# Optimization experiments

Hardware: AMD Instinct MI355X
Metric: run time of the kernel (lower is better)

The kernel has to match this reference:

```python
import jax, jax.numpy as jnp
import numpy as np

B, H, KVH, D = 32, 32, 8, 128
BS = 128                      # KV-cache block size
BLOCKS_PER_SEQ = 14
NB = B * BLOCKS_PER_SEQ       # 448 active blocks
NUM_CACHE_BLOCKS = 512
CTX = 13 * BS + 64            # 1728 tokens per sequence (incl. new decode token)
SCALE = 0.08838834764831845   # 1/sqrt(head_size)
NEG = -1e9


def _slopes(n):
    return (2.0 ** (-8.0 / n * np.arange(1, n + 1))).astype(np.float32)


def setup_inputs() -> dict:
    key = jax.random.key(0)
    ks = jax.random.split(key, 5)
    query = jax.random.normal(ks[0], (B, 1, H * D), dtype=jnp.float32)
    key_t = jax.random.normal(ks[1], (B, 1, KVH * D), dtype=jnp.float32)
    value = jax.random.normal(ks[2], (B, 1, KVH * D), dtype=jnp.float32)
    key_cache = jax.random.normal(ks[3], (NUM_CACHE_BLOCKS, BS, KVH, D), dtype=jnp.float32)
    value_cache = jax.random.normal(ks[4], (NUM_CACHE_BLOCKS, BS, KVH, D), dtype=jnp.float32)

    block_list = np.arange(NB, dtype=np.int32)                      # cache block id per active block (seq-major)
    block_groups = np.repeat(np.arange(B, dtype=np.int32), BLOCKS_PER_SEQ)
    block_mapping = np.zeros((NB, B), dtype=np.float32)             # one-hot block->batch map
    block_mapping[np.arange(NB), block_groups] = 1.0

    valid = CTX - 13 * BS                                           # 64 valid slots in last block
    block_bias = np.zeros((NB, BS), dtype=np.float32)
    last = np.arange(B) * BLOCKS_PER_SEQ + (BLOCKS_PER_SEQ - 1)
    block_bias[last, valid:] = NEG

    # alibi distances per kv slot: (kv_pos - (CTX-1)); zero on masked slots
    pos_in_seq = (np.tile(np.arange(BLOCKS_PER_SEQ), B)[:, None] * BS
                  + np.arange(BS)[None, :]).astype(np.float32)
    alibi_blocks = np.where(block_bias < 0, 0.0, pos_in_seq - float(CTX - 1)).astype(np.float32)

    block_indices = last.astype(np.int32)                           # write new token into last block
    block_offsets = np.full((B,), valid - 1, dtype=np.int32)

    return {"query": query, "key": key_t, "value": value,
            "key_cache": key_cache, "value_cache": value_cache,
            "block_list": jnp.asarray(block_list), "block_groups": jnp.asarray(block_groups),
            "block_mapping": jnp.asarray(block_mapping), "block_bias": jnp.asarray(block_bias),
            "block_indices": jnp.asarray(block_indices), "block_offsets": jnp.asarray(block_offsets),
            "alibi_blocks": jnp.asarray(alibi_blocks), "alibi_slopes": jnp.asarray(_slopes(H))}


def reference(query, key, value, key_cache, value_cache, block_list, block_groups,
              block_mapping, block_bias, block_indices, block_offsets,
              alibi_blocks, alibi_slopes):
    G = H // KVH                                                    # queries per kv head
    q = query.reshape(B, H, D)
    k_new = key.reshape(B, KVH, D)
    v_new = value.reshape(B, KVH, D)
    # KV-cache insertion of the new decode token (VLLMKVCache insert)
    key_cache = key_cache.at[block_indices, block_offsets].set(k_new)
    value_cache = value_cache.at[block_indices, block_offsets].set(v_new)
    # batch2block: replicate each sequence's query to its blocks via one-hot matmul
    q_blk = jnp.einsum('nb,bhd->nhd', block_mapping, SCALE * q).reshape(NB, KVH, G, D)
    k = key_cache[block_list]                                       # [NB, BS, KVH, D] paged fetch
    v = value_cache[block_list]
    attn = jnp.einsum('nkgd,nskd->nkgs', q_blk, k)                  # [NB, KVH, G, BS]
    # decode alibi bias: slopes * per-slot distance, grouped for GQA
    pos_bias = (alibi_blocks[:, None, :] * alibi_slopes[None, :, None]).reshape(NB, KVH, G, BS)
    attn = attn + pos_bias + block_bias[:, None, None, :]
    # grouped (per-sequence) numerically-stable softmax across blocks
    block_max = jnp.max(attn, axis=-1)                              # [NB, KVH, G]
    group_max = jax.ops.segment_max(block_max, block_groups, num_segments=B)
    m = jax.lax.stop_gradient(group_max[block_groups])
    p = jnp.exp(attn - m[..., None])
    block_sum = jnp.sum(p, axis=-1)                                 # [NB, KVH, G]
    o_blk = jnp.einsum('nkgs,nskd->nkgd', p, v)                     # [NB, KVH, G, D]
    # block2batch: accumulate block partials back per sequence
    o = jnp.einsum('nb,nkgd->bkgd', block_mapping, o_blk)
    s = jnp.einsum('nb,nkg->bkg', block_mapping, block_sum)
    out = o / s[..., None]
    return out.reshape(B, 1, H * D)
```

## Files before the change

kernel.cpp:

```cpp
#include <hip/hip_runtime.h>
#include <stdint.h>

#define B_    32
#define H_    32
#define KVH_  8
#define D_    128
#define BS_   128
#define BPS_  14
#define NB_   448
#define G_    4
#define CHUNK_ 32
#define SCALE_ 0.08838834764831845f

__device__ __forceinline__ void g2lds16(const float* gp, float* lp) {
  __builtin_amdgcn_global_load_lds(
      (__attribute__((address_space(1))) void*)gp,
      (__attribute__((address_space(3))) void*)lp,
      16, 0, 0);
}

__global__ __launch_bounds__(256, 4) void attn_part_kernel(
    const float* __restrict__ query,
    const float* __restrict__ knew, const float* __restrict__ vnew,
    const float* __restrict__ kc, const float* __restrict__ vc,
    const int* __restrict__ block_list, const int* __restrict__ block_groups,
    const float* __restrict__ block_bias, const float* __restrict__ alibi_blocks,
    const float* __restrict__ alibi_slopes,
    float* __restrict__ p_o, float* __restrict__ p_m, float* __restrict__ p_l) {
  __shared__ float smem[2 * CHUNK_ * D_];
  __shared__ float q_s[G_ * D_];
  __shared__ float attn_s[G_ * BS_];
  __shared__ float bias_s[BS_];
  __shared__ float alibi_s[BS_];

  const int bid = blockIdx.x;
  const int n = bid >> 3, kvh = bid & 7;
  const int t = threadIdx.x;
  const int lane = t & 63, wv = t >> 6;
  const int s_loc = lane & 31, dh = lane >> 5;

  const int cb = block_list[n];
  const int b  = block_groups[n];
  const bool is_last = (n % BPS_ == BPS_ - 1);
  const int nch = is_last ? 2 : 4;

  const float* kbase = kc + ((size_t)cb * BS_ * KVH_ + kvh) * D_;
  const float* vbase = vc + ((size_t)cb * BS_ * KVH_ + kvh) * D_;
  const float* knew_row = knew + ((size_t)b * KVH_ + kvh) * D_;
  const float* vnew_row = vnew + ((size_t)b * KVH_ + kvh) * D_;

  {
    int r = wv * 8;
    #pragma unroll
    for (int i = 0; i < 4; ++i) {
      const float* g = kbase + (size_t)(r + 2 * i + dh) * (KVH_ * D_) + s_loc * 4;
      g2lds16(g, smem + (r + 2 * i) * D_);
    }
  }
  if (t < 128) {
    float4 qv = *(const float4*)(query + (size_t)b * (H_ * D_) +
                                 (size_t)kvh * (G_ * D_) + (size_t)t * 4);
    qv.x *= SCALE_; qv.y *= SCALE_; qv.z *= SCALE_; qv.w *= SCALE_;
    ((float4*)q_s)[t] = qv;
  } else {
    int i = t - 128;
    bias_s[i]  = block_bias[(size_t)n * BS_ + i];
    alibi_s[i] = alibi_blocks[(size_t)n * BS_ + i];
  }
  const float slope = alibi_slopes[kvh * G_ + wv];
  __syncthreads();

  const int rot = s_loc & 15;

  for (int c = 0; c < nch; ++c) {
    if (c + 1 < nch) {
      float* dst = smem + ((c + 1) & 1) * (CHUNK_ * D_);
      int r = wv * 8;
      #pragma unroll
      for (int i = 0; i < 4; ++i) {
        int row = (c + 1) * CHUNK_ + r + 2 * i + dh;
        const float* g = (is_last && row == 63)
                             ? knew_row + s_loc * 4
                             : kbase + (size_t)row * (KVH_ * D_) + s_loc * 4;
        g2lds16(g, dst + (r + 2 * i) * D_);
      }
    }
    float acc = 0.f;
    const float4* kb = (const float4*)(smem + (c & 1) * (CHUNK_ * D_) + s_loc * D_ + dh * 64);
    const float4* qb = (const float4*)(q_s + wv * D_ + dh * 64);
    #pragma unroll
    for (int j = 0; j < 16; ++j) {
      int jj = (j + rot) & 15;
      float4 kvv = kb[jj];
      float4 qv = qb[jj];
      acc += kvv.x * qv.x + kvv.y * qv.y + kvv.z * qv.z + kvv.w * qv.w;
    }
    acc += __shfl_xor(acc, 32);
    if (lane < 32) {
      int s = c * CHUNK_ + s_loc;
      attn_s[wv * BS_ + s] = acc + slope * alibi_s[s] + bias_s[s];
    }
    __syncthreads();
  }

  {
    float a0 = attn_s[wv * BS_ + lane];
    float a1 = (nch == 4) ? attn_s[wv * BS_ + 64 + lane] : -1e30f;
    float mx = fmaxf(a0, a1);
    #pragma unroll
    for (int off = 32; off > 0; off >>= 1) mx = fmaxf(mx, __shfl_xor(mx, off));
    float p0 = __expf(a0 - mx);
    float p1 = __expf(a1 - mx);
    attn_s[wv * BS_ + lane] = p0;
    if (nch == 4) attn_s[wv * BS_ + 64 + lane] = p1;
    float sm = p0 + p1;
    #pragma unroll
    for (int off = 32; off > 0; off >>= 1) sm += __shfl_xor(sm, off);
    if (lane == 0) {
      p_m[(size_t)bid * G_ + wv] = mx;
      p_l[(size_t)bid * G_ + wv] = sm;
    }
  }
  __syncthreads();

  const int col4 = (lane & 31) * 4;
  const int group = wv * 2 + (lane >> 5);
  float4 acc4[G_];
  #pragma unroll
  for (int g = 0; g < G_; ++g) acc4[g] = make_float4(0.f, 0.f, 0.f, 0.f);

  if (group < nch * 2) {
    #pragma unroll
    for (int half = 0; half < 2; ++half) {
      float4 v4[8];
      #pragma unroll
      for (int i = 0; i < 8; ++i) {
        int s = group * 16 + half * 8 + i;
        const float* src = (is_last && s == 63)
                               ? vnew_row + col4
                               : vbase + (size_t)s * (KVH_ * D_) + col4;
        v4[i] = *(const float4*)src;
      }
      #pragma unroll
      for (int i = 0; i < 8; ++i) {
        int s = group * 16 + half * 8 + i;
        #pragma unroll
        for (int g = 0; g < G_; ++g) {
          float pg = attn_s[g * BS_ + s];
          acc4[g].x += pg * v4[i].x;
          acc4[g].y += pg * v4[i].y;
          acc4[g].z += pg * v4[i].z;
          acc4[g].w += pg * v4[i].w;
        }
      }
    }
  }

  float* red = smem;
  {
    #pragma unroll
    for (int g = 0; g < G_; ++g)
      *(float4*)&red[group * (G_ * D_) + g * D_ + col4] = acc4[g];
  }
  __syncthreads();
  {
    int g = t >> 6;
    int d = (t & 63) * 2;
    float2 sum = make_float2(0.f, 0.f);
    #pragma unroll
    for (int w = 0; w < 8; ++w) {
      float2 r = *(const float2*)&red[w * (G_ * D_) + g * D_ + d];
      sum.x += r.x; sum.y += r.y;
    }
    *(float2*)(p_o + ((size_t)bid * G_ + g) * D_ + d) = sum;
  }
}

__global__ __launch_bounds__(256) void attn_reduce_kernel(
    const float* __restrict__ p_o, const float* __restrict__ p_m,
    const float* __restrict__ p_l, float* __restrict__ out) {
  int bk = blockIdx.x;
  int b = bk >> 3, kvh = bk & 7;
  int t = threadIdx.x;
  int g = t >> 6, lane = t & 63;
  int d = lane * 2;

  float M = -1e30f;
  #pragma unroll
  for (int i = 0; i < BPS_; ++i) {
    size_t pid = ((size_t)(b * BPS_ + i) * KVH_ + kvh) * G_ + g;
    M = fmaxf(M, p_m[pid]);
  }
  float denom = 0.f;
  float2 acc = make_float2(0.f, 0.f);
  #pragma unroll
  for (int i = 0; i < BPS_; ++i) {
    size_t pid = ((size_t)(b * BPS_ + i) * KVH_ + kvh) * G_ + g;
    float w = __expf(p_m[pid] - M);
    denom += w * p_l[pid];
    float2 o = *(const float2*)(p_o + pid * D_ + d);
    acc.x += w * o.x;
    acc.y += w * o.y;
  }
  float inv = 1.f / denom;
  float2 r = make_float2(acc.x * inv, acc.y * inv);
  *(float2*)(out + (size_t)b * (H_ * D_) + (size_t)(kvh * G_ + g) * D_ + d) = r;
}

extern "C" void kernel_launch(void* const* d_in, const int* in_sizes, int n_in,
                              void* d_out, int out_size, void* d_ws, size_t ws_size,
                              hipStream_t stream) {
  const float* query = (const float*)d_in[0];
  const float* key   = (const float*)d_in[1];
  const float* value = (const float*)d_in[2];
  const float* kc    = (const float*)d_in[3];
  const float* vc    = (const float*)d_in[4];
  const int* block_list    = (const int*)d_in[5];
  const int* block_groups  = (const int*)d_in[6];
  const float* block_bias  = (const float*)d_in[8];
  const float* alibi_blocks = (const float*)d_in[11];
  const float* alibi_slopes = (const float*)d_in[12];
  float* out = (float*)d_out;

  const size_t n_po = (size_t)NB_ * KVH_ * G_ * D_;
  const size_t n_pm = (size_t)NB_ * KVH_ * G_;
  float* p_o = (float*)d_ws;
  float* p_m = p_o + n_po;
  float* p_l = p_m + n_pm;

  attn_part_kernel<<<NB_ * KVH_, 256, 0, stream>>>(
      query, key, value, kc, vc, block_list, block_groups, block_bias,
      alibi_blocks, alibi_slopes, p_o, p_m, p_l);
  attn_reduce_kernel<<<B_ * KVH_, 256, 0, stream>>>(p_o, p_m, p_l, out);
}
```

Measured before the change: 519.7 us.

## Fuse split-KV reduction into partial kernel via last-block-arrives atomic counter

```diff
diff --git a/kernel.cpp b/kernel.cpp
--- a/kernel.cpp
+++ b/kernel.cpp
@@ -19,19 +19,21 @@
       16, 0, 0);
 }
 
-__global__ __launch_bounds__(256, 4) void attn_part_kernel(
+__global__ __launch_bounds__(256, 4) void attn_fused_kernel(
     const float* __restrict__ query,
     const float* __restrict__ knew, const float* __restrict__ vnew,
     const float* __restrict__ kc, const float* __restrict__ vc,
     const int* __restrict__ block_list, const int* __restrict__ block_groups,
     const float* __restrict__ block_bias, const float* __restrict__ alibi_blocks,
     const float* __restrict__ alibi_slopes,
-    float* __restrict__ p_o, float* __restrict__ p_m, float* __restrict__ p_l) {
+    float* __restrict__ p_o, float* __restrict__ p_m, float* __restrict__ p_l,
+    unsigned int* __restrict__ cnt, float* __restrict__ out) {
   __shared__ float smem[2 * CHUNK_ * D_];
   __shared__ float q_s[G_ * D_];
   __shared__ float attn_s[G_ * BS_];
   __shared__ float bias_s[BS_];
   __shared__ float alibi_s[BS_];
+  __shared__ unsigned int s_arrival;
 
   const int bid = blockIdx.x;
   const int n = bid >> 3, kvh = bid & 7;
@@ -174,37 +176,39 @@
     }
     *(float2*)(p_o + ((size_t)bid * G_ + g) * D_ + d) = sum;
   }
-}
-
-__global__ __launch_bounds__(256) void attn_reduce_kernel(
-    const float* __restrict__ p_o, const float* __restrict__ p_m,
-    const float* __restrict__ p_l, float* __restrict__ out) {
-  int bk = blockIdx.x;
-  int b = bk >> 3, kvh = bk & 7;
-  int t = threadIdx.x;
-  int g = t >> 6, lane = t & 63;
-  int d = lane * 2;
-
-  float M = -1e30f;
-  #pragma unroll
-  for (int i = 0; i < BPS_; ++i) {
-    size_t pid = ((size_t)(b * BPS_ + i) * KVH_ + kvh) * G_ + g;
-    M = fmaxf(M, p_m[pid]);
-  }
-  float denom = 0.f;
-  float2 acc = make_float2(0.f, 0.f);
-  #pragma unroll
-  for (int i = 0; i < BPS_; ++i) {
-    size_t pid = ((size_t)(b * BPS_ + i) * KVH_ + kvh) * G_ + g;
-    float w = __expf(p_m[pid] - M);
-    denom += w * p_l[pid];
-    float2 o = *(const float2*)(p_o + pid * D_ + d);
-    acc.x += w * o.x;
-    acc.y += w * o.y;
-  }
-  float inv = 1.f / denom;
-  float2 r = make_float2(acc.x * inv, acc.y * inv);
-  *(float2*)(out + (size_t)b * (H_ * D_) + (size_t)(kvh * G_ + g) * D_ + d) = r;
+
+  __syncthreads();
+  const int bk = b * KVH_ + kvh;
+  if (t == 0) {
+    __threadfence();
+    s_arrival = atomicAdd(&cnt[bk], 1u);
+  }
+  __syncthreads();
+  if (s_arrival == BPS_ - 1) {
+    __threadfence();
+    int g = t >> 6;
+    int d = (t & 63) * 2;
+    float M = -1e30f;
+    #pragma unroll
+    for (int i = 0; i < BPS_; ++i) {
+      size_t pid = ((size_t)(b * BPS_ + i) * KVH_ + kvh) * G_ + g;
+      M = fmaxf(M, p_m[pid]);
+    }
+    float denom = 0.f;
+    float2 acc = make_float2(0.f, 0.f);
+    #pragma unroll
+    for (int i = 0; i < BPS_; ++i) {
+      size_t pid = ((size_t)(b * BPS_ + i) * KVH_ + kvh) * G_ + g;
+      float w = __expf(p_m[pid] - M);
+      denom += w * p_l[pid];
+      float2 o = *(const float2*)(p_o + pid * D_ + d);
+      acc.x += w * o.x;
+      acc.y += w * o.y;
+    }
+    float inv = 1.f / denom;
+    *(float2*)(out + (size_t)b * (H_ * D_) + (size_t)(kvh * G_ + g) * D_ + d) =
+        make_float2(acc.x * inv, acc.y * inv);
+  }
 }
 
 extern "C" void kernel_launch(void* const* d_in, const int* in_sizes, int n_in,
@@ -227,9 +231,11 @@
   float* p_o = (float*)d_ws;
   float* p_m = p_o + n_po;
   float* p_l = p_m + n_pm;
-
-  attn_part_kernel<<<NB_ * KVH_, 256, 0, stream>>>(
+  unsigned int* cnt = (unsigned int*)(p_l + n_pm);
+
+  hipMemsetAsync(cnt, 0, (size_t)B_ * KVH_ * sizeof(unsigned int), stream);
+
+  attn_fused_kernel<<<NB_ * KVH_, 256, 0, stream>>>(
       query, key, value, kc, vc, block_list, block_groups, block_bias,
-      alibi_blocks, alibi_slopes, p_o, p_m, p_l);
-  attn_reduce_kernel<<<B_ * KVH_, 256, 0, stream>>>(p_o, p_m, p_l, out);
+      alibi_blocks, alibi_slopes, p_o, p_m, p_l, cnt, out);
 }
```

New measurement: 740.3 us. 1.42x slower.
